# Kernel tuning notes

Hardware: AMD Instinct MI355X
Metric: run time of the kernel (lower is better)

Reference implementation:

```python
import jax, jax.numpy as jnp
import numpy as np

N_NODES = 1_000_000
N_EDGES = 16_000_000


def setup_inputs() -> dict:
    key = jax.random.key(0)
    k1, k2, k3, k4 = jax.random.split(key, 4)
    x = jax.random.normal(k1, (N_NODES, 2), dtype=jnp.float32)
    edge_index = jax.random.randint(k2, (2, N_EDGES), 0, N_NODES, dtype=jnp.int64)
    W1 = jax.random.normal(k3, (2, 4), dtype=jnp.float32) * 0.5
    b1 = jnp.zeros((4,), dtype=jnp.float32)
    W2 = jax.random.normal(k4, (4, 2), dtype=jnp.float32) * 0.5
    b2 = jnp.zeros((2,), dtype=jnp.float32)
    return {"x": x, "edge_index": edge_index, "W1": W1, "b1": b1, "W2": W2, "b2": b2}


def _gcn_conv(h, src, dst, norm, b, n_nodes):
    # h already linearly transformed: message = h[src] * norm, scatter-add to dst
    msg = h[src] * norm[:, None]
    out = jax.ops.segment_sum(msg, dst, num_segments=n_nodes)
    return out + b


def reference(x, edge_index, W1, b1, W2, b2):
    n = x.shape[0]
    loop = jnp.arange(n, dtype=edge_index.dtype)
    # PyG GCNConv default: add self-loops, symmetric deg^{-1/2} normalization
    src = jnp.concatenate([edge_index[0], loop])
    dst = jnp.concatenate([edge_index[1], loop])
    deg = jax.ops.segment_sum(jnp.ones_like(src, dtype=x.dtype), dst, num_segments=n)
    dinv = jnp.where(deg > 0, jax.lax.rsqrt(deg), 0.0)
    norm = dinv[src] * dinv[dst]

    h = _gcn_conv(x @ W1, src, dst, norm, b1, n)   # conv1: [N,2] -> [N,4]
    h = jax.nn.relu(h)
    out = _gcn_conv(h @ W2, src, dst, norm, b2, n)  # conv2: [N,4] -> [N,2]
    return out
```

## Files before the change

### kernel.cpp

```cpp
#include <hip/hip_runtime.h>
#include <hip/hip_fp16.h>


constexpr int W_SHIFT = 11;
constexpr int W = 2048;
constexpr int MAXB = 512;
constexpr int RB = 1024;
constexpr int CHUNK = 8192;
constexpr int AB = 512;

constexpr float SCALE1 = 65536.0f;
constexpr float INV1   = 1.0f / 65536.0f;
constexpr unsigned BIAS1 = 1u << 20;
constexpr float SCALE2 = 4096.0f;
constexpr float INV2   = 1.0f / 4096.0f;
constexpr unsigned BIAS2 = 1u << 22;

typedef unsigned uv4 __attribute__((ext_vector_type(4)));
typedef int      iv4 __attribute__((ext_vector_type(4)));

__device__ __forceinline__ unsigned long long pack2(float a, float b,
                                                    float scale, unsigned bias) {
    unsigned lo = (unsigned)(__float2int_rn(a * scale) + (int)bias);
    unsigned hi = (unsigned)(__float2int_rn(b * scale) + (int)bias);
    return (unsigned long long)lo | ((unsigned long long)hi << 32);
}

__global__ __launch_bounds__(256) void k_zero_fill(unsigned* __restrict__ fill,
                                                   int nb, unsigned C) {
    int i = blockIdx.x * 256 + threadIdx.x;
    if (i < nb) fill[i] = (unsigned)i * C;
}

__global__ __launch_bounds__(RB) void k_reorder(const int* __restrict__ src,
                                                const int* __restrict__ dst,
                                                unsigned* __restrict__ fill,
                                                unsigned* __restrict__ perm, int E) {
    __shared__ unsigned hist[MAXB];
    __shared__ unsigned lbase[MAXB];
    __shared__ unsigned gdelta[MAXB];
    __shared__ unsigned sorted[CHUNK];
    __shared__ unsigned short sbb[CHUNK];
    int tid = threadIdx.x;
    if (tid < MAXB) hist[tid] = 0u;
    __syncthreads();
    long base0 = (long)blockIdx.x * CHUNK;
    int total = (int)min((long)CHUNK, (long)E - base0);
    bool full = (total == CHUNK);

    if (full) {
        const iv4* dv4 = (const iv4*)(dst + base0);
        #pragma unroll
        for (int k = 0; k < 2; k++) {
            iv4 q = dv4[k * RB + tid];
            atomicAdd(&hist[((unsigned)q.x) >> W_SHIFT], 1u);
            atomicAdd(&hist[((unsigned)q.y) >> W_SHIFT], 1u);
            atomicAdd(&hist[((unsigned)q.z) >> W_SHIFT], 1u);
            atomicAdd(&hist[((unsigned)q.w) >> W_SHIFT], 1u);
        }
    } else {
        for (int li = tid; li < total; li += RB)
            atomicAdd(&hist[((unsigned)dst[base0 + li]) >> W_SHIFT], 1u);
    }
    __syncthreads();
    unsigned v = (tid < MAXB) ? hist[tid] : 0u;
    if (tid < MAXB) lbase[tid] = v;
    __syncthreads();
    for (int off = 1; off < MAXB; off <<= 1) {
        unsigned u = (tid >= off && tid < MAXB) ? lbase[tid - off] : 0u;
        __syncthreads();
        if (tid < MAXB) lbase[tid] += u;
        __syncthreads();
    }
    if (tid < MAXB) {
        unsigned excl = lbase[tid] - v;
        unsigned gd = 0u;
        if (v) gd = atomicAdd(&fill[tid], v) - excl;
        gdelta[tid] = gd;
        hist[tid] = excl;
    }
    __syncthreads();
    if (full) {
        const iv4* dv4 = (const iv4*)(dst + base0);
        const iv4* sv4 = (const iv4*)(src + base0);
        #pragma unroll
        for (int k = 0; k < 2; k++) {
            iv4 dq = dv4[k * RB + tid];
            iv4 sq = sv4[k * RB + tid];
            unsigned d, b, lpos;
            d = (unsigned)dq.x; b = d >> W_SHIFT; lpos = atomicAdd(&hist[b], 1u);
            sorted[lpos] = (unsigned)sq.x | ((d & (W - 1)) << 20); sbb[lpos] = (unsigned short)b;
            d = (unsigned)dq.y; b = d >> W_SHIFT; lpos = atomicAdd(&hist[b], 1u);
            sorted[lpos] = (unsigned)sq.y | ((d & (W - 1)) << 20); sbb[lpos] = (unsigned short)b;
            d = (unsigned)dq.z; b = d >> W_SHIFT; lpos = atomicAdd(&hist[b], 1u);
            sorted[lpos] = (unsigned)sq.z | ((d & (W - 1)) << 20); sbb[lpos] = (unsigned short)b;
            d = (unsigned)dq.w; b = d >> W_SHIFT; lpos = atomicAdd(&hist[b], 1u);
            sorted[lpos] = (unsigned)sq.w | ((d & (W - 1)) << 20); sbb[lpos] = (unsigned short)b;
        }
    } else {
        for (int li = tid; li < total; li += RB) {
            unsigned d = (unsigned)dst[base0 + li];
            unsigned s = (unsigned)src[base0 + li];
            unsigned b = d >> W_SHIFT;
            unsigned lpos = atomicAdd(&hist[b], 1u);
            sorted[lpos] = s | ((d & (W - 1)) << 20);
            sbb[lpos] = (unsigned short)b;
        }
    }
    __syncthreads();
    if (full) {
        #pragma unroll
        for (int k = 0; k < CHUNK / RB; k++) {
            int t = k * RB + tid;
            unsigned b = sbb[t];
            perm[gdelta[b] + t] = sorted[t];
        }
    } else {
        for (int t = tid; t < total; t += RB) {
            unsigned b = sbb[t];
            perm[gdelta[b] + t] = sorted[t];
        }
    }
}

__global__ __launch_bounds__(AB) void k_dinv(const unsigned* __restrict__ perm,
                                             const unsigned* __restrict__ fill,
                                             const float2* __restrict__ x,
                                             float* __restrict__ dinv,
                                             unsigned* __restrict__ deg,
                                             __half2* __restrict__ xs,
                                             int N, unsigned C) {
    __shared__ unsigned c[2 * W];
    for (int i = threadIdx.x; i < 2 * W; i += AB) c[i] = 0u;
    __syncthreads();
    int b = blockIdx.x;
    unsigned par = threadIdx.x & 1u;
    unsigned s = (unsigned)b * C, e = fill[b];
    unsigned m = e - s, nv8 = m >> 3;
    const uv4* p4 = (const uv4*)(perm + s);
    for (unsigned j = threadIdx.x; j < nv8; j += AB) {
        uv4 qa = __builtin_nontemporal_load(p4 + 2u * j);
        uv4 qb = __builtin_nontemporal_load(p4 + 2u * j + 1u);
        atomicAdd(&c[((qa.x >> 20) << 1) | par], 1u);
        atomicAdd(&c[((qa.y >> 20) << 1) | par], 1u);
        atomicAdd(&c[((qa.z >> 20) << 1) | par], 1u);
        atomicAdd(&c[((qa.w >> 20) << 1) | par], 1u);
        atomicAdd(&c[((qb.x >> 20) << 1) | par], 1u);
        atomicAdd(&c[((qb.y >> 20) << 1) | par], 1u);
        atomicAdd(&c[((qb.z >> 20) << 1) | par], 1u);
        atomicAdd(&c[((qb.w >> 20) << 1) | par], 1u);
    }
    unsigned t = s + (nv8 << 3) + threadIdx.x;
    if (t < e) atomicAdd(&c[((perm[t] >> 20) << 1) | par], 1u);
    __syncthreads();
    int d0 = b << W_SHIFT;
    for (int l = threadIdx.x; l < W; l += AB) {
        int d = d0 + l;
        if (d < N) {
            unsigned cn = c[2 * l] + c[2 * l + 1];
            float dv = 1.0f / sqrtf((float)(cn + 1u));
            dinv[d] = dv;
            deg[d] = cn;
            float2 xv = x[d];
            xs[d] = __floats2half2_rn(xv.x * dv, xv.y * dv);
        }
    }
}

__global__ __launch_bounds__(AB) void k_acc1(const unsigned* __restrict__ perm,
                                             const unsigned* __restrict__ fill,
                                             const __half2* __restrict__ xs,
                                             const float* __restrict__ dinv,
                                             const unsigned* __restrict__ deg,
                                             const float* __restrict__ W1,
                                             const float* __restrict__ b1,
                                             const float* __restrict__ W2,
                                             __half2* __restrict__ h2s,
                                             int N, unsigned C) {
    __shared__ unsigned long long acc[2 * W];
    for (int i = threadIdx.x; i < 2 * W; i += AB) acc[i] = 0ull;
    __syncthreads();
    int b = blockIdx.x;
    unsigned par = threadIdx.x & 1u;
    unsigned s = (unsigned)b * C, e = fill[b];
    unsigned m = e - s, nv8 = m >> 3;
    const uv4* p4 = (const uv4*)(perm + s);
    for (unsigned j = threadIdx.x; j < nv8; j += AB) {
        uv4 qa = __builtin_nontemporal_load(p4 + 2u * j);
        uv4 qb = __builtin_nontemporal_load(p4 + 2u * j + 1u);
        float2 v0 = __half22float2(xs[qa.x & 0xFFFFFu]);
        float2 v1 = __half22float2(xs[qa.y & 0xFFFFFu]);
        float2 v2 = __half22float2(xs[qa.z & 0xFFFFFu]);
        float2 v3 = __half22float2(xs[qa.w & 0xFFFFFu]);
        float2 v4 = __half22float2(xs[qb.x & 0xFFFFFu]);
        float2 v5 = __half22float2(xs[qb.y & 0xFFFFFu]);
        float2 v6 = __half22float2(xs[qb.z & 0xFFFFFu]);
        float2 v7 = __half22float2(xs[qb.w & 0xFFFFFu]);
        atomicAdd(&acc[((qa.x >> 20) << 1) | par], pack2(v0.x, v0.y, SCALE1, BIAS1));
        atomicAdd(&acc[((qa.y >> 20) << 1) | par], pack2(v1.x, v1.y, SCALE1, BIAS1));
        atomicAdd(&acc[((qa.z >> 20) << 1) | par], pack2(v2.x, v2.y, SCALE1, BIAS1));
        atomicAdd(&acc[((qa.w >> 20) << 1) | par], pack2(v3.x, v3.y, SCALE1, BIAS1));
        atomicAdd(&acc[((qb.x >> 20) << 1) | par], pack2(v4.x, v4.y, SCALE1, BIAS1));
        atomicAdd(&acc[((qb.y >> 20) << 1) | par], pack2(v5.x, v5.y, SCALE1, BIAS1));
        atomicAdd(&acc[((qb.z >> 20) << 1) | par], pack2(v6.x, v6.y, SCALE1, BIAS1));
        atomicAdd(&acc[((qb.w >> 20) << 1) | par], pack2(v7.x, v7.y, SCALE1, BIAS1));
    }
    unsigned t = s + (nv8 << 3) + threadIdx.x;
    if (t < e) {
        unsigned p = perm[t];
        float2 v = __half22float2(xs[p & 0xFFFFFu]);
        atomicAdd(&acc[((p >> 20) << 1) | par], pack2(v.x, v.y, SCALE1, BIAS1));
    }
    __syncthreads();
    int d0 = b << W_SHIFT;
    float w10 = W1[0], w11 = W1[1], w12 = W1[2], w13 = W1[3];
    float w14 = W1[4], w15 = W1[5], w16 = W1[6], w17 = W1[7];
    float bb0 = b1[0], bb1 = b1[1], bb2 = b1[2], bb3 = b1[3];
    float u0 = W2[0], u1 = W2[1], u2 = W2[2], u3 = W2[3];
    float u4 = W2[4], u5 = W2[5], u6 = W2[6], u7 = W2[7];
    for (int l = threadIdx.x; l < W; l += AB) {
        int d = d0 + l;
        if (d < N) {
            float dv = dinv[d];
            unsigned cn = deg[d];
            unsigned long long a64 = acc[2 * l] + acc[2 * l + 1];
            unsigned lo = (unsigned)a64, hi = (unsigned)(a64 >> 32);
            float2 self = __half22float2(xs[d]);
            float Sx = (float)(int)(lo - cn * BIAS1) * INV1 + self.x;
            float Sy = (float)(int)(hi - cn * BIAS1) * INV1 + self.y;
            float a0 = fmaxf(fmaf(Sy, w14, Sx * w10) * dv + bb0, 0.0f);
            float a1 = fmaxf(fmaf(Sy, w15, Sx * w11) * dv + bb1, 0.0f);
            float a2 = fmaxf(fmaf(Sy, w16, Sx * w12) * dv + bb2, 0.0f);
            float a3 = fmaxf(fmaf(Sy, w17, Sx * w13) * dv + bb3, 0.0f);
            float hx = (a0 * u0 + a1 * u2 + a2 * u4 + a3 * u6) * dv;
            float hy = (a0 * u1 + a1 * u3 + a2 * u5 + a3 * u7) * dv;
            h2s[d] = __floats2half2_rn(hx, hy);
        }
    }
}

__global__ __launch_bounds__(AB) void k_acc2(const unsigned* __restrict__ perm,
                                             const unsigned* __restrict__ fill,
                                             const __half2* __restrict__ h2s,
                                             const float* __restrict__ dinv,
                                             const unsigned* __restrict__ deg,
                                             const float* __restrict__ b2,
                                             float2* __restrict__ out,
                                             int N, unsigned C) {
    __shared__ unsigned long long acc[2 * W];
    for (int i = threadIdx.x; i < 2 * W; i += AB) acc[i] = 0ull;
    __syncthreads();
    int b = blockIdx.x;
    unsigned par = threadIdx.x & 1u;
    unsigned s = (unsigned)b * C, e = fill[b];
    unsigned m = e - s, nv8 = m >> 3;
    const uv4* p4 = (const uv4*)(perm + s);
    for (unsigned j = threadIdx.x; j < nv8; j += AB) {
        uv4 qa = __builtin_nontemporal_load(p4 + 2u * j);
        uv4 qb = __builtin_nontemporal_load(p4 + 2u * j + 1u);
        float2 v0 = __half22float2(h2s[qa.x & 0xFFFFFu]);
        float2 v1 = __half22float2(h2s[qa.y & 0xFFFFFu]);
        float2 v2 = __half22float2(h2s[qa.z & 0xFFFFFu]);
        float2 v3 = __half22float2(h2s[qa.w & 0xFFFFFu]);
        float2 v4 = __half22float2(h2s[qb.x & 0xFFFFFu]);
        float2 v5 = __half22float2(h2s[qb.y & 0xFFFFFu]);
        float2 v6 = __half22float2(h2s[qb.z & 0xFFFFFu]);
        float2 v7 = __half22float2(h2s[qb.w & 0xFFFFFu]);
        atomicAdd(&acc[((qa.x >> 20) << 1) | par], pack2(v0.x, v0.y, SCALE2, BIAS2));
        atomicAdd(&acc[((qa.y >> 20) << 1) | par], pack2(v1.x, v1.y, SCALE2, BIAS2));
        atomicAdd(&acc[((qa.z >> 20) << 1) | par], pack2(v2.x, v2.y, SCALE2, BIAS2));
        atomicAdd(&acc[((qa.w >> 20) << 1) | par], pack2(v3.x, v3.y, SCALE2, BIAS2));
        atomicAdd(&acc[((qb.x >> 20) << 1) | par], pack2(v4.x, v4.y, SCALE2, BIAS2));
        atomicAdd(&acc[((qb.y >> 20) << 1) | par], pack2(v5.x, v5.y, SCALE2, BIAS2));
        atomicAdd(&acc[((qb.z >> 20) << 1) | par], pack2(v6.x, v6.y, SCALE2, BIAS2));
        atomicAdd(&acc[((qb.w >> 20) << 1) | par], pack2(v7.x, v7.y, SCALE2, BIAS2));
    }
    unsigned t = s + (nv8 << 3) + threadIdx.x;
    if (t < e) {
        unsigned p = perm[t];
        float2 v = __half22float2(h2s[p & 0xFFFFFu]);
        atomicAdd(&acc[((p >> 20) << 1) | par], pack2(v.x, v.y, SCALE2, BIAS2));
    }
    __syncthreads();
    int d0 = b << W_SHIFT;
    float bb0 = b2[0], bb1 = b2[1];
    for (int l = threadIdx.x; l < W; l += AB) {
        int d = d0 + l;
        if (d < N) {
            float dv = dinv[d];
            unsigned cn = deg[d];
            unsigned long long a64 = acc[2 * l] + acc[2 * l + 1];
            unsigned lo = (unsigned)a64, hi = (unsigned)(a64 >> 32);
            float2 v = __half22float2(h2s[d]);
            float Sx = (float)(int)(lo - cn * BIAS2) * INV2 + v.x;
            float Sy = (float)(int)(hi - cn * BIAS2) * INV2 + v.y;
            out[d] = make_float2(Sx * dv + bb0, Sy * dv + bb1);
        }
    }
}


__global__ __launch_bounds__(256) void f_init_deg(unsigned* deg, int n) {
    int i = blockIdx.x * 256 + threadIdx.x;
    if (i < n) deg[i] = 1u;
}
__global__ __launch_bounds__(256) void f_count_deg(const int* dst, unsigned* deg, int E) {
    int e = blockIdx.x * 256 + threadIdx.x;
    if (e < E) atomicAdd(&deg[dst[e]], 1u);
}
__global__ __launch_bounds__(256) void f_node1(const float2* x, const float* W1,
                                               const unsigned* deg, float* dinv,
                                               float4* h1s, float4* agg1, int n) {
    int i = blockIdx.x * 256 + threadIdx.x;
    if (i >= n) return;
    float dv = 1.0f / sqrtf((float)deg[i]);
    dinv[i] = dv;
    float2 xv = x[i];
    float4 h;
    h.x = fmaf(xv.y, W1[4], xv.x * W1[0]) * dv;
    h.y = fmaf(xv.y, W1[5], xv.x * W1[1]) * dv;
    h.z = fmaf(xv.y, W1[6], xv.x * W1[2]) * dv;
    h.w = fmaf(xv.y, W1[7], xv.x * W1[3]) * dv;
    h1s[i] = h;
    agg1[i] = make_float4(h.x * dv, h.y * dv, h.z * dv, h.w * dv);
}
__global__ __launch_bounds__(256) void f_edge1(const int* src, const int* dst,
                                               const float* dinv, const float4* h1s,
                                               float* agg1, int E) {
    int e = blockIdx.x * 256 + threadIdx.x;
    if (e >= E) return;
    int s = src[e], d = dst[e];
    float w = dinv[d];
    float4 m = h1s[s];
    float* p = agg1 + 4ll * d;
    unsafeAtomicAdd(p + 0, m.x * w);
    unsafeAtomicAdd(p + 1, m.y * w);
    unsafeAtomicAdd(p + 2, m.z * w);
    unsafeAtomicAdd(p + 3, m.w * w);
}
__global__ __launch_bounds__(256) void f_node2(const float4* agg1, const float* b1,
                                               const float* W2, const float* b2,
                                               const float* dinv, float2* h2s,
                                               float2* out, int n) {
    int i = blockIdx.x * 256 + threadIdx.x;
    if (i >= n) return;
    float4 a = agg1[i];
    a.x = fmaxf(a.x + b1[0], 0.0f);
    a.y = fmaxf(a.y + b1[1], 0.0f);
    a.z = fmaxf(a.z + b1[2], 0.0f);
    a.w = fmaxf(a.w + b1[3], 0.0f);
    float dv = dinv[i];
    float2 h;
    h.x = (a.x * W2[0] + a.y * W2[2] + a.z * W2[4] + a.w * W2[6]) * dv;
    h.y = (a.x * W2[1] + a.y * W2[3] + a.z * W2[5] + a.w * W2[7]) * dv;
    h2s[i] = h;
    out[i] = make_float2(b2[0] + h.x * dv, b2[1] + h.y * dv);
}
__global__ __launch_bounds__(256) void f_edge2(const int* src, const int* dst,
                                               const float* dinv, const float2* h2s,
                                               float* out, int E) {
    int e = blockIdx.x * 256 + threadIdx.x;
    if (e >= E) return;
    int s = src[e], d = dst[e];
    float w = dinv[d];
    float2 m = h2s[s];
    float* p = out + 2ll * d;
    unsafeAtomicAdd(p + 0, m.x * w);
    unsafeAtomicAdd(p + 1, m.y * w);
}

extern "C" void kernel_launch(void* const* d_in, const int* in_sizes, int n_in,
                              void* d_out, int out_size, void* d_ws, size_t ws_size,
                              hipStream_t stream) {
    const float* x  = (const float*)d_in[0];
    const int* ei   = (const int*)d_in[1];
    const float* W1 = (const float*)d_in[2];
    const float* b1 = (const float*)d_in[3];
    const float* W2 = (const float*)d_in[4];
    const float* b2 = (const float*)d_in[5];
    float* out = (float*)d_out;

    const int N = in_sizes[0] / 2;
    const int E = in_sizes[1] / 2;
    const int* src = ei;
    const int* dst = ei + E;
    const int NB = (N + W - 1) >> W_SHIFT;

    char* ws = (char*)d_ws;
    const int gN = (N + 255) / 256;
    const int gE = (E + 255) / 256;

    size_t fixed = 32768 + (size_t)16 * N;
    long avail = (long)ws_size - (long)fixed;
    long Cmax = (avail > 0) ? avail / (4L * NB) : 0;
    long Cmin = (long)(E / (NB > 0 ? NB : 1)) + 4096;
    long Cw = (Cmax > Cmin + 8192) ? (Cmin + 8192) : Cmax;
    unsigned C = (unsigned)(Cw & ~7L);
    bool fast = ((long)C >= Cmin) && (NB <= MAXB) && (N <= (1 << 20));

    if (fast) {
        unsigned* fill = (unsigned*)(ws);
        float*    dinv = (float*)(ws + 32768);
        unsigned* deg  = (unsigned*)(ws + 32768 + (size_t)4 * N);
        __half2*  xs   = (__half2*)(ws + 32768 + (size_t)8 * N);
        __half2*  h2s  = (__half2*)(ws + 32768 + (size_t)12 * N);
        unsigned* perm = (unsigned*)(ws + fixed);

        k_zero_fill<<<(NB + 255) / 256, 256, 0, stream>>>(fill, NB, C);
        k_reorder<<<(E + CHUNK - 1) / CHUNK, RB, 0, stream>>>(src, dst, fill, perm, E);
        k_dinv<<<NB, AB, 0, stream>>>(perm, fill, (const float2*)x, dinv, deg, xs, N, C);
        k_acc1<<<NB, AB, 0, stream>>>(perm, fill, xs, dinv, deg, W1, b1, W2, h2s, N, C);
        k_acc2<<<NB, AB, 0, stream>>>(perm, fill, h2s, dinv, deg, b2, (float2*)out, N, C);
    } else {
        unsigned* deg = (unsigned*)(ws);
        float* dinv   = (float*)(ws + (size_t)4 * N);
        float* h1s    = (float*)(ws + (size_t)8 * N);
        float* agg1   = (float*)(ws + (size_t)24 * N);
        float* h2s    = h1s;

        f_init_deg<<<gN, 256, 0, stream>>>(deg, N);
        f_count_deg<<<gE, 256, 0, stream>>>(dst, deg, E);
        f_node1<<<gN, 256, 0, stream>>>((const float2*)x, W1, deg, dinv,
                                        (float4*)h1s, (float4*)agg1, N);
        f_edge1<<<gE, 256, 0, stream>>>(src, dst, dinv, (const float4*)h1s, agg1, E);
        f_node2<<<gN, 256, 0, stream>>>((const float4*)agg1, b1, W2, b2, dinv,
                                        (float2*)h2s, (float2*)out, N);
        f_edge2<<<gE, 256, 0, stream>>>(src, dst, dinv, (const float2*)h2s, out, E);
    }
}
```

Measured before the change: 434.0 us.

## Fuse degree counting into reorder via global atomics, replace dinv pass with node kernel

Degree counting moves into the reorder kernel, which now does a global atomic increment per edge on a per-node degree array. This removes the separate k_dinv pass that re-read the whole permuted edge buffer to build shared-memory histograms. A simple per-node kernel then computes dinv and the scaled features, and the fill counters become relative offsets that are zeroed with memsets. The trade-off is 16M random global atomics scattered over a 4MB array in exchange for skipping one full streaming pass over perm.

New measurement: 972.3 us. 2.24x slower.

```diff
diff --git a/kernel.cpp b/kernel.cpp
--- a/kernel.cpp
+++ b/kernel.cpp
@@ -26,16 +26,12 @@
     return (unsigned long long)lo | ((unsigned long long)hi << 32);
 }
 
-__global__ __launch_bounds__(256) void k_zero_fill(unsigned* __restrict__ fill,
-                                                   int nb, unsigned C) {
-    int i = blockIdx.x * 256 + threadIdx.x;
-    if (i < nb) fill[i] = (unsigned)i * C;
-}
-
 __global__ __launch_bounds__(RB) void k_reorder(const int* __restrict__ src,
                                                 const int* __restrict__ dst,
                                                 unsigned* __restrict__ fill,
-                                                unsigned* __restrict__ perm, int E) {
+                                                unsigned* __restrict__ perm,
+                                                unsigned* __restrict__ deg,
+                                                int E, unsigned C) {
     __shared__ unsigned hist[MAXB];
     __shared__ unsigned lbase[MAXB];
     __shared__ unsigned gdelta[MAXB];
@@ -57,10 +53,17 @@
             atomicAdd(&hist[((unsigned)q.y) >> W_SHIFT], 1u);
             atomicAdd(&hist[((unsigned)q.z) >> W_SHIFT], 1u);
             atomicAdd(&hist[((unsigned)q.w) >> W_SHIFT], 1u);
+            atomicAdd(&deg[(unsigned)q.x], 1u);
+            atomicAdd(&deg[(unsigned)q.y], 1u);
+            atomicAdd(&deg[(unsigned)q.z], 1u);
+            atomicAdd(&deg[(unsigned)q.w], 1u);
         }
     } else {
-        for (int li = tid; li < total; li += RB)
-            atomicAdd(&hist[((unsigned)dst[base0 + li]) >> W_SHIFT], 1u);
+        for (int li = tid; li < total; li += RB) {
+            unsigned d = (unsigned)dst[base0 + li];
+            atomicAdd(&hist[d >> W_SHIFT], 1u);
+            atomicAdd(&deg[d], 1u);
+        }
     }
     __syncthreads();
     unsigned v = (tid < MAXB) ? hist[tid] : 0u;
@@ -75,7 +78,7 @@
     if (tid < MAXB) {
         unsigned excl = lbase[tid] - v;
         unsigned gd = 0u;
-        if (v) gd = atomicAdd(&fill[tid], v) - excl;
+        if (v) gd = (unsigned)tid * C + atomicAdd(&fill[tid], v) - excl;
         gdelta[tid] = gd;
         hist[tid] = excl;
     }
@@ -123,48 +126,16 @@
     }
 }
 
-__global__ __launch_bounds__(AB) void k_dinv(const unsigned* __restrict__ perm,
-                                             const unsigned* __restrict__ fill,
-                                             const float2* __restrict__ x,
-                                             float* __restrict__ dinv,
-                                             unsigned* __restrict__ deg,
-                                             __half2* __restrict__ xs,
-                                             int N, unsigned C) {
-    __shared__ unsigned c[2 * W];
-    for (int i = threadIdx.x; i < 2 * W; i += AB) c[i] = 0u;
-    __syncthreads();
-    int b = blockIdx.x;
-    unsigned par = threadIdx.x & 1u;
-    unsigned s = (unsigned)b * C, e = fill[b];
-    unsigned m = e - s, nv8 = m >> 3;
-    const uv4* p4 = (const uv4*)(perm + s);
-    for (unsigned j = threadIdx.x; j < nv8; j += AB) {
-        uv4 qa = __builtin_nontemporal_load(p4 + 2u * j);
-        uv4 qb = __builtin_nontemporal_load(p4 + 2u * j + 1u);
-        atomicAdd(&c[((qa.x >> 20) << 1) | par], 1u);
-        atomicAdd(&c[((qa.y >> 20) << 1) | par], 1u);
-        atomicAdd(&c[((qa.z >> 20) << 1) | par], 1u);
-        atomicAdd(&c[((qa.w >> 20) << 1) | par], 1u);
-        atomicAdd(&c[((qb.x >> 20) << 1) | par], 1u);
-        atomicAdd(&c[((qb.y >> 20) << 1) | par], 1u);
-        atomicAdd(&c[((qb.z >> 20) << 1) | par], 1u);
-        atomicAdd(&c[((qb.w >> 20) << 1) | par], 1u);
-    }
-    unsigned t = s + (nv8 << 3) + threadIdx.x;
-    if (t < e) atomicAdd(&c[((perm[t] >> 20) << 1) | par], 1u);
-    __syncthreads();
-    int d0 = b << W_SHIFT;
-    for (int l = threadIdx.x; l < W; l += AB) {
-        int d = d0 + l;
-        if (d < N) {
-            unsigned cn = c[2 * l] + c[2 * l + 1];
-            float dv = 1.0f / sqrtf((float)(cn + 1u));
-            dinv[d] = dv;
-            deg[d] = cn;
-            float2 xv = x[d];
-            xs[d] = __floats2half2_rn(xv.x * dv, xv.y * dv);
-        }
-    }
+__global__ __launch_bounds__(256) void k_node(const unsigned* __restrict__ deg,
+                                              const float2* __restrict__ x,
+                                              float* __restrict__ dinv,
+                                              __half2* __restrict__ xs, int n) {
+    int i = blockIdx.x * 256 + threadIdx.x;
+    if (i >= n) return;
+    float dv = 1.0f / sqrtf((float)(deg[i] + 1u));
+    dinv[i] = dv;
+    float2 xv = x[i];
+    xs[i] = __floats2half2_rn(xv.x * dv, xv.y * dv);
 }
 
 __global__ __launch_bounds__(AB) void k_acc1(const unsigned* __restrict__ perm,
@@ -182,7 +153,7 @@
     __syncthreads();
     int b = blockIdx.x;
     unsigned par = threadIdx.x & 1u;
-    unsigned s = (unsigned)b * C, e = fill[b];
+    unsigned s = (unsigned)b * C, e = s + fill[b];
     unsigned m = e - s, nv8 = m >> 3;
     const uv4* p4 = (const uv4*)(perm + s);
     for (unsigned j = threadIdx.x; j < nv8; j += AB) {
@@ -252,7 +223,7 @@
     __syncthreads();
     int b = blockIdx.x;
     unsigned par = threadIdx.x & 1u;
-    unsigned s = (unsigned)b * C, e = fill[b];
+    unsigned s = (unsigned)b * C, e = s + fill[b];
     unsigned m = e - s, nv8 = m >> 3;
     const uv4* p4 = (const uv4*)(perm + s);
     for (unsigned j = threadIdx.x; j < nv8; j += AB) {
@@ -406,9 +377,11 @@
         __half2*  h2s  = (__half2*)(ws + 32768 + (size_t)12 * N);
         unsigned* perm = (unsigned*)(ws + fixed);
 
-        k_zero_fill<<<(NB + 255) / 256, 256, 0, stream>>>(fill, NB, C);
-        k_reorder<<<(E + CHUNK - 1) / CHUNK, RB, 0, stream>>>(src, dst, fill, perm, E);
-        k_dinv<<<NB, AB, 0, stream>>>(perm, fill, (const float2*)x, dinv, deg, xs, N, C);
+        hipMemsetAsync(fill, 0, (size_t)NB * 4, stream);
+        hipMemsetAsync(deg, 0, (size_t)N * 4, stream);
+        k_reorder<<<(E + CHUNK - 1) / CHUNK, RB, 0, stream>>>(src, dst, fill, perm,
+                                                              deg, E, C);
+        k_node<<<gN, 256, 0, stream>>>(deg, (const float2*)x, dinv, xs, N);
         k_acc1<<<NB, AB, 0, stream>>>(perm, fill, xs, dinv, deg, W1, b1, W2, h2s, N, C);
         k_acc2<<<NB, AB, 0, stream>>>(perm, fill, h2s, dinv, deg, b2, (float2*)out, N, C);
     } else {
```
